# Kernel optimization log

Measured on AMD Instinct MI355X. Metric: run time of the kernel, lower is better.

## Reference

```python
import jax, jax.numpy as jnp
import numpy as np
from jax.scipy.special import digamma

# Dims (see init_kwargs): pose P=4 -> D=16, stem A=128, primary caps B=32,
# classes C=10, class-caps kernel K=6 (== primary feature map size), 3 routing iters.
P, D, A, B, C, K, ITER = 4, 16, 128, 32, 10, 6, 3
N = B * K * K                                    # input capsules routed to each class capsule
ALPHA0, KAPPA0, NU0 = 1.0, 1.0, float(D + 1)     # Dirichlet/Normal-Wishart priors (m0=0, Psi0=I, cov='diag')
BN_EPS, EPS = 1e-5, 1e-8


def conv2d(x, w, s):
    return jax.lax.conv_general_dilated(x, w, (s, s), 'VALID',
                                        dimension_numbers=('NCHW', 'OIHW', 'NCHW'))


def bn(x, gamma, beta, axes):
    # batch-norm with batch statistics (training-mode math)
    mu = x.mean(axes, keepdims=True)
    var = x.var(axes, keepdims=True)
    return (x - mu) * jax.lax.rsqrt(var + BN_EPS) * gamma + beta


def setup_inputs():
    key = jax.random.key(0)
    ks = jax.random.split(key, 4)
    f32 = jnp.float32
    x = jax.random.normal(ks[0], (128, 3, 32, 32), dtype=f32)
    conv1_w = jax.random.normal(ks[1], (A, 3, 5, 5), dtype=f32) * 0.1
    bn1_g = jnp.ones((A,), f32); bn1_b = jnp.zeros((A,), f32)
    prim_w = jax.random.normal(ks[2], (B * D + B, A, 3, 3), dtype=f32) * 0.05
    bna_g = jnp.ones((B,), f32); bna_b = jnp.zeros((B,), f32)
    bnp_g = jnp.ones((B,), f32); bnp_b = jnp.zeros((B,), f32)
    W_ij = jax.random.normal(ks[3], (B, C, K, K, P, P), dtype=f32) * 0.3
    return dict(x=x, conv1_w=conv1_w, bn1_g=bn1_g, bn1_b=bn1_b, prim_w=prim_w,
                bna_g=bna_g, bna_b=bna_b, bnp_g=bnp_g, bnp_b=bnp_b, W_ij=W_ij)


def _vb_stats(Ra, V):
    # Ra: (b,N,C) responsibility * input activation; V: (b,N,C,D) votes
    Nj = Ra.sum(1) + EPS                                         # (b,C)
    xbar = jnp.einsum('bnc,bncd->bcd', Ra, V) / Nj[..., None]    # weighted vote mean
    diff = V - xbar[:, None]
    sigma = jnp.einsum('bnc,bncd->bcd', Ra, diff * diff) / Nj[..., None]  # diag cov
    kappa = KAPPA0 + Nj
    m = Nj[..., None] * xbar / kappa[..., None]                  # posterior mean (m0 = 0)
    nu = NU0 + Nj
    Psi = 1.0 + Nj[..., None] * sigma + (KAPPA0 * Nj / kappa)[..., None] * xbar * xbar  # Psi0 = I (diag)
    return Nj, kappa, m, nu, Psi


def _expectations(Nj, nu, Psi, d_idx):
    alpha = ALPHA0 + Nj
    E_lnpi = digamma(alpha) - digamma(alpha.sum(-1, keepdims=True))
    E_lnLam = (digamma(0.5 * (nu[..., None] + 1.0 - d_idx)).sum(-1)
               + D * jnp.log(2.0) - jnp.log(Psi).sum(-1))
    return E_lnpi, E_lnLam


def reference(x, conv1_w, bn1_g, bn1_b, prim_w, bna_g, bna_b, bnp_g, bnp_b, W_ij):
    b = x.shape[0]
    # --- stem: Conv5x5/s2 + BN + ReLU ---
    h = conv2d(x, conv1_w, 2)                                    # (b,A,14,14)
    h = jax.nn.relu(bn(h, bn1_g[None, :, None, None], bn1_b[None, :, None, None], (0, 2, 3)))
    # --- primary capsules: Conv3x3/s2 -> poses + activations ---
    pc = conv2d(h, prim_w, 2)                                    # (b,B*D+B,6,6)
    poses, a = pc[:, :B * D], pc[:, B * D:]
    a = jax.nn.sigmoid(bn(a, bna_g[None, :, None, None], bna_b[None, :, None, None], (0, 2, 3)))
    poses = bn(poses.reshape(b, B, D, K, K),
               bnp_g[None, :, None, None, None], bnp_b[None, :, None, None, None], (0, 2, 3, 4))
    poses = poses.reshape(b, B, P, P, K, K)
    # --- class capsules: votes V = W_ij @ pose, kernel covers whole 6x6 map ---
    V = jnp.einsum('icxypq,biqrxy->bicxypr', W_ij, poses)        # (b,B,C,K,K,P,P)
    V = V.transpose(0, 1, 3, 4, 2, 5, 6).reshape(b, N, C, D)
    a_i = a.reshape(b, N)
    # --- variational Bayes routing (diag Normal-Wishart, ITER iterations) ---
    d_idx = jnp.arange(1, D + 1, dtype=x.dtype)
    R = jnp.full((b, N, C), 1.0 / C, dtype=x.dtype)
    for t in range(ITER):
        Nj, kappa, m, nu, Psi = _vb_stats(R * a_i[:, :, None], V)
        if t < ITER - 1:
            E_lnpi, E_lnLam = _expectations(Nj, nu, Psi, d_idx)
            dm = V - m[:, None]
            quad = D / kappa[:, None, :] + nu[:, None, :] * jnp.einsum('bncd,bcd->bnc', dm * dm, 1.0 / Psi)
            lnp = (E_lnpi[:, None] + 0.5 * E_lnLam[:, None]
                   - 0.5 * D * jnp.log(2.0 * jnp.pi) - 0.5 * quad)
            R = jax.nn.softmax(lnp, axis=-1)
    E_lnpi, E_lnLam = _expectations(Nj, nu, Psi, d_idx)
    logits = E_lnpi + 0.5 * E_lnLam                              # (b,C)
    yhat = jax.nn.sigmoid(bn(logits, 1.0, 0.0, (0,)))            # BatchNorm1d(affine=False)
    return yhat
```

## Files before the change

kernel.cpp:

```cpp
#include <hip/hip_runtime.h>
#include <hip/hip_bf16.h>

#define NB 128
#define AA 128
#define BB 32
#define CC 10
#define KK 6
#define DD 16
#define NN 1152
#define H1 14
#define CH2 544
#define NG 4608
#define KG 1152
#define MG 576

typedef short bfrag8 __attribute__((ext_vector_type(8)));
typedef float facc4 __attribute__((ext_vector_type(4)));

__device__ __forceinline__ unsigned short f2bf(float f) {
    unsigned u = __float_as_uint(f);
    u += 0x7FFF + ((u >> 16) & 1);
    return (unsigned short)(u >> 16);
}
__device__ __forceinline__ float bf2f(unsigned short s) {
    return __uint_as_float(((unsigned)s) << 16);
}

__global__ __launch_bounds__(256, 3) void k_conv1(const float* __restrict__ x,
                                                  const float* __restrict__ w,
                                                  float* __restrict__ h) {
    __shared__ __align__(16) float sX[3][7][32];
    __shared__ float sWf[AA * 75];
    const int p = blockIdx.x;
    const int b = blockIdx.y;
    const int tid = threadIdx.x;
    for (int j = tid; j < AA * 75; j += 256) sWf[j] = w[j];
    for (int j = tid; j < 3 * 7 * 32; j += 256) {
        int col = j & 31; int t2 = j >> 5; int row = t2 % 7; int ic = t2 / 7;
        sX[ic][row][col] = x[b * 3072 + ic * 1024 + (4 * p + row) * 32 + col];
    }
    __syncthreads();
    const int oc = tid & 127, ry = tid >> 7;
    const int r = 2 * p + ry;
    float acc[14];
#pragma unroll
    for (int j = 0; j < 14; ++j) acc[j] = 0.f;
    const float* wr = sWf + oc * 75;
#pragma unroll
    for (int ic = 0; ic < 3; ++ic) {
#pragma unroll
        for (int ky = 0; ky < 5; ++ky) {
            const float* xr = &sX[ic][2 * ry + ky][0];
            float row[32];
#pragma unroll
            for (int q = 0; q < 8; ++q) {
                float4 v = *reinterpret_cast<const float4*>(xr + q * 4);
                row[q * 4 + 0] = v.x; row[q * 4 + 1] = v.y;
                row[q * 4 + 2] = v.z; row[q * 4 + 3] = v.w;
            }
            float w0 = wr[ic * 25 + ky * 5 + 0];
            float w1 = wr[ic * 25 + ky * 5 + 1];
            float w2 = wr[ic * 25 + ky * 5 + 2];
            float w3 = wr[ic * 25 + ky * 5 + 3];
            float w4 = wr[ic * 25 + ky * 5 + 4];
#pragma unroll
            for (int ox = 0; ox < 14; ++ox) {
                float s = acc[ox];
                s = fmaf(row[2 * ox + 0], w0, s);
                s = fmaf(row[2 * ox + 1], w1, s);
                s = fmaf(row[2 * ox + 2], w2, s);
                s = fmaf(row[2 * ox + 3], w3, s);
                s = fmaf(row[2 * ox + 4], w4, s);
                acc[ox] = s;
            }
        }
    }
    float* out = h + ((size_t)(b * AA + oc) * 14 + r) * 14;
#pragma unroll
    for (int q = 0; q < 7; ++q)
        *reinterpret_cast<float2*>(out + q * 2) = make_float2(acc[q * 2], acc[q * 2 + 1]);
}

__device__ __forceinline__ void blk_reduce2(float& s, float& s2, int tid) {
#pragma unroll
    for (int o = 32; o > 0; o >>= 1) { s += __shfl_down(s, o); s2 += __shfl_down(s2, o); }
    __shared__ float ls[4], lq[4];
    int lane = tid & 63, wid = tid >> 6;
    if (lane == 0) { ls[wid] = s; lq[wid] = s2; }
    __syncthreads();
    if (tid == 0) {
        s = ls[0] + ls[1] + ls[2] + ls[3];
        s2 = lq[0] + lq[1] + lq[2] + lq[3];
    }
}

__global__ void k_bnstats1a(const float* __restrict__ h, float* __restrict__ part) {
    int c = blockIdx.x & 127, sl = blockIdx.x >> 7;
    int tid = threadIdx.x;
    float s = 0.f, s2 = 0.f;
    for (int j = tid; j < 16 * 196; j += 256) {
        int b = sl * 16 + j / 196, hw = j % 196;
        float v = h[((size_t)b * AA + c) * 196 + hw];
        s += v; s2 += v * v;
    }
    blk_reduce2(s, s2, tid);
    if (tid == 0) { part[c * 8 + sl] = s; part[1024 + c * 8 + sl] = s2; }
}

__global__ void k_bnfin1(const float* __restrict__ part, const float* __restrict__ g,
                         const float* __restrict__ be, float* __restrict__ bn1) {
    int c = threadIdx.x;
    float s = 0.f, s2 = 0.f;
#pragma unroll
    for (int sl = 0; sl < 8; ++sl) { s += part[c * 8 + sl]; s2 += part[1024 + c * 8 + sl]; }
    const float n = (float)(NB * 196);
    float mu = s / n;
    float var = s2 / n - mu * mu;
    float sc = g[c] * rsqrtf(var + 1e-5f);
    bn1[c] = sc;
    bn1[AA + c] = be[c] - mu * sc;
}

__global__ void k_prepw(const float* __restrict__ w, unsigned short* __restrict__ Ah,
                        unsigned short* __restrict__ Al) {
    int t = blockIdx.x * 256 + threadIdx.x;
    if (t >= MG * (KG / 8)) return;
    int row = t / (KG / 8), seg = t % (KG / 8);
    alignas(16) unsigned short hi[8], lo[8];
    if (row < CH2) {
        const float* src = w + (size_t)row * KG + seg * 8;
#pragma unroll
        for (int j = 0; j < 8; ++j) {
            float v = src[j];
            unsigned short hh = f2bf(v);
            hi[j] = hh;
            lo[j] = f2bf(v - bf2f(hh));
        }
    } else {
#pragma unroll
        for (int j = 0; j < 8; ++j) { hi[j] = 0; lo[j] = 0; }
    }
    *reinterpret_cast<uint4*>(Ah + (size_t)row * KG + seg * 8) = *reinterpret_cast<const uint4*>(hi);
    *reinterpret_cast<uint4*>(Al + (size_t)row * KG + seg * 8) = *reinterpret_cast<const uint4*>(lo);
}

__global__ void k_im2col(const float* __restrict__ h, const float* __restrict__ bn1,
                         unsigned short* __restrict__ Bh, unsigned short* __restrict__ Bl) {
    int t = blockIdx.x * 256 + threadIdx.x;
    if (t >= NG * (KG / 8)) return;
    int n = t / (KG / 8), seg = t % (KG / 8);
    int b = n / 36, xy = n % 36;
    int oy = xy / 6, ox = xy % 6;
    const float* hb = h + (size_t)b * (AA * 196) + (2 * oy) * 14 + 2 * ox;
    alignas(16) unsigned short hi[8], lo[8];
#pragma unroll
    for (int j = 0; j < 8; ++j) {
        int k = seg * 8 + j;
        int ic = k / 9, kk = k - ic * 9;
        int ky = kk / 3, kx = kk - ky * 3;
        float v = hb[ic * 196 + ky * 14 + kx];
        v = fmaxf(fmaf(v, bn1[ic], bn1[AA + ic]), 0.f);
        unsigned short hh = f2bf(v);
        hi[j] = hh;
        lo[j] = f2bf(v - bf2f(hh));
    }
    *reinterpret_cast<uint4*>(Bh + (size_t)n * KG + seg * 8) = *reinterpret_cast<const uint4*>(hi);
    *reinterpret_cast<uint4*>(Bl + (size_t)n * KG + seg * 8) = *reinterpret_cast<const uint4*>(lo);
}

__global__ __launch_bounds__(256, 4) void k_gemm(const unsigned short* __restrict__ Ah,
                                                 const unsigned short* __restrict__ Al,
                                                 const unsigned short* __restrict__ Bh,
                                                 const unsigned short* __restrict__ Bl,
                                                 float* __restrict__ pcT) {
    __shared__ alignas(16) unsigned short sAh[64][44], sAl[64][44];
    __shared__ alignas(16) unsigned short sBh[64][44], sBl[64][44];
    const int s = blockIdx.x;
    const int k8 = s & 7, j = s >> 3;
    const int jm = j / 9;
    const int y = k8 + 8 * jm;
    const int xg = j - 9 * jm;
    const int oc0 = xg * 64;
    const int n0 = y * 64;
    const int tid = threadIdx.x;
    const int lane = tid & 63, wv = tid >> 6;
    const int wm = wv >> 1, wn = wv & 1;
    const int quad = lane >> 4, r16 = lane & 15;
    const int srow = tid >> 2, sseg = tid & 3;

    facc4 acc[2][2] = {};
    const size_t gA = (size_t)(oc0 + srow) * KG + sseg * 8;
    const size_t gB = (size_t)(n0 + srow) * KG + sseg * 8;

    for (int ks = 0; ks < KG / 32; ++ks) {
        const int k0 = ks * 32;
        uint4 vAh = *reinterpret_cast<const uint4*>(Ah + gA + k0);
        uint4 vAl = *reinterpret_cast<const uint4*>(Al + gA + k0);
        uint4 vBh = *reinterpret_cast<const uint4*>(Bh + gB + k0);
        uint4 vBl = *reinterpret_cast<const uint4*>(Bl + gB + k0);
        __syncthreads();
        *reinterpret_cast<uint4*>(&sAh[srow][sseg * 8]) = vAh;
        *reinterpret_cast<uint4*>(&sAl[srow][sseg * 8]) = vAl;
        *reinterpret_cast<uint4*>(&sBh[srow][sseg * 8]) = vBh;
        *reinterpret_cast<uint4*>(&sBl[srow][sseg * 8]) = vBl;
        __syncthreads();
        bfrag8 ah[2], al[2], bh[2], bl[2];
#pragma unroll
        for (int i = 0; i < 2; ++i) {
            ah[i] = *reinterpret_cast<const bfrag8*>(&sAh[wm * 32 + i * 16 + r16][quad * 8]);
            al[i] = *reinterpret_cast<const bfrag8*>(&sAl[wm * 32 + i * 16 + r16][quad * 8]);
            bh[i] = *reinterpret_cast<const bfrag8*>(&sBh[wn * 32 + i * 16 + r16][quad * 8]);
            bl[i] = *reinterpret_cast<const bfrag8*>(&sBl[wn * 32 + i * 16 + r16][quad * 8]);
        }
#pragma unroll
        for (int i = 0; i < 2; ++i)
#pragma unroll
            for (int jj = 0; jj < 2; ++jj) {
                acc[i][jj] = __builtin_amdgcn_mfma_f32_16x16x32_bf16(ah[i], bh[jj], acc[i][jj], 0, 0, 0);
                acc[i][jj] = __builtin_amdgcn_mfma_f32_16x16x32_bf16(ah[i], bl[jj], acc[i][jj], 0, 0, 0);
                acc[i][jj] = __builtin_amdgcn_mfma_f32_16x16x32_bf16(al[i], bh[jj], acc[i][jj], 0, 0, 0);
            }
    }
#pragma unroll
    for (int i = 0; i < 2; ++i) {
        int oc_base = oc0 + wm * 32 + i * 16 + quad * 4;
        if (oc_base >= CH2) continue;
#pragma unroll
        for (int jj = 0; jj < 2; ++jj) {
            int n = n0 + wn * 32 + jj * 16 + r16;
            *reinterpret_cast<facc4*>(pcT + (size_t)n * CH2 + oc_base) = acc[i][jj];
        }
    }
}

__global__ void k_bnstats2a(const float* __restrict__ pcT, float* __restrict__ part) {
    int blk = blockIdx.x, tid = threadIdx.x;
    float s = 0.f, s2 = 0.f;
    if (blk < 256) {
        int i = blk >> 3, sl = blk & 7;
        for (int j = tid; j < 576 * 4; j += 256) {
            int row = sl * 576 + (j >> 2), q = j & 3;
            float4 v = *reinterpret_cast<const float4*>(pcT + (size_t)row * CH2 + i * 16 + q * 4);
            s += v.x + v.y + v.z + v.w;
            s2 += v.x * v.x + v.y * v.y + v.z * v.z + v.w * v.w;
        }
        blk_reduce2(s, s2, tid);
        if (tid == 0) { part[blk] = s; part[256 + blk] = s2; }
    } else {
        int t2 = blk - 256;
        int ch = t2 >> 1, sl = t2 & 1;
        for (int j = tid; j < 2304; j += 256) {
            int row = sl * 2304 + j;
            float v = pcT[(size_t)row * CH2 + BB * DD + ch];
            s += v; s2 += v * v;
        }
        blk_reduce2(s, s2, tid);
        if (tid == 0) { part[512 + t2] = s; part[576 + t2] = s2; }
    }
}

__global__ void k_bnfin2(const float* __restrict__ part,
                         const float* __restrict__ bna_g, const float* __restrict__ bna_b,
                         const float* __restrict__ bnp_g, const float* __restrict__ bnp_b,
                         float* __restrict__ bn2) {
    int t = threadIdx.x;
    if (t < 32) {
        float s = 0.f, s2 = 0.f;
#pragma unroll
        for (int sl = 0; sl < 8; ++sl) { s += part[t * 8 + sl]; s2 += part[256 + t * 8 + sl]; }
        const float n = (float)(NB * DD * 36);
        float mu = s / n, var = s2 / n - mu * mu;
        float sc = bnp_g[t] * rsqrtf(var + 1e-5f);
        bn2[t] = sc; bn2[32 + t] = bnp_b[t] - mu * sc;
    } else {
        int ch = t - 32;
        float s = part[512 + ch * 2] + part[512 + ch * 2 + 1];
        float s2 = part[576 + ch * 2] + part[576 + ch * 2 + 1];
        const float n = (float)(NB * 36);
        float mu = s / n, var = s2 / n - mu * mu;
        float sc = bna_g[ch] * rsqrtf(var + 1e-5f);
        bn2[64 + ch] = sc; bn2[96 + ch] = bna_b[ch] - mu * sc;
    }
}

__device__ __forceinline__ float digammaf_(float x) {
    float r = 0.f;
    while (x < 6.f) { r -= 1.f / x; x += 1.f; }
    float xi = 1.f / x;
    float xi2 = xi * xi;
    return r + logf(x) - 0.5f * xi -
           xi2 * (0.0833333333f - xi2 * (0.0083333333f - xi2 * 0.0039682540f));
}

template <int FIRST>
__global__ __launch_bounds__(640) void k_routed(
    const float* __restrict__ pcT, const float* __restrict__ bn2,
    const float* __restrict__ Wij,
    const float* __restrict__ S0i, const float* __restrict__ S1i, const float* __restrict__ S2i,
    float* __restrict__ S0o, float* __restrict__ S1o, float* __restrict__ S2o) {
    const int b = blockIdx.x >> 1, half = blockIdx.x & 1;
    const int tid = threadIdx.x;
    const int c = tid >> 6, lane = tid & 63;
    __shared__ float sLnp[CC][66];
    __shared__ float sBn2[128];
    __shared__ __align__(16) float sP[64][20];
    __shared__ float sA[64];
    __shared__ float sM[CC][16], sGq[CC][16], sBase[CC];
    if (tid < 128) sBn2[tid] = bn2[tid];
    if (!FIRST && tid < 160) {
        int cc = tid >> 4, d = tid & 15;
        int bc = b * CC + cc;
        float njraw = S0i[bc] + S0i[NB * CC + bc];
        float nj = njraw + 1e-8f;
        float kappa = 1.f + nj;
        float nu = 17.f + nj;
        float s1 = S1i[bc * 16 + d] + S1i[(NB * CC + bc) * 16 + d];
        float s2v = S2i[bc * 16 + d] + S2i[(NB * CC + bc) * 16 + d];
        float xbar = s1 / nj;
        float sig = (s2v - 2.f * xbar * s1 + xbar * xbar * njraw) / nj;
        float Psi = 1.f + nj * sig + (nj / kappa) * xbar * xbar;
        sM[cc][d] = nj * xbar / kappa;
        sGq[cc][d] = 0.5f * nu / Psi;
        float term = digammaf_(0.5f * (nu + 1.f - (float)(d + 1))) - logf(Psi);
#pragma unroll
        for (int o = 8; o > 0; o >>= 1) term += __shfl_down(term, o, 16);
        if (d == 0) {
            float asum = 0.f;
#pragma unroll
            for (int k = 0; k < CC; ++k)
                asum += 1.f + S0i[b * CC + k] + S0i[NB * CC + b * CC + k] + 1e-8f;
            float elnlam = 16.f * 0.69314718056f + term;
            float elnpi = digammaf_(1.f + nj) - digammaf_(asum);
            float lb = elnpi + 0.5f * elnlam;
            sBase[cc] = lb - 8.f * 1.83787706641f - 8.f / kappa;
        }
    }
    __syncthreads();
    float mc[16], Gc[16], basec = 0.f;
    if (!FIRST) {
#pragma unroll
        for (int d = 0; d < 16; ++d) { mc[d] = sM[c][d]; Gc[d] = sGq[c][d]; }
        basec = sBase[c];
    }
    float s0 = 0.f, s1[16], s2[16];
#pragma unroll
    for (int d = 0; d < 16; ++d) { s1[d] = 0.f; s2[d] = 0.f; }

#pragma unroll 1
    for (int it = 0; it < 9; ++it) {
        if (tid < 256) {
            int r = tid >> 2, q = tid & 3;
            int n = half * 576 + it * 64 + r;
            int i = n / 36, xy = n - i * 36;
            int row = b * 36 + xy;
            float4 v = *reinterpret_cast<const float4*>(pcT + (size_t)row * CH2 + i * 16 + q * 4);
            float psc = sBn2[i], psh = sBn2[32 + i];
            v.x = fmaf(v.x, psc, psh); v.y = fmaf(v.y, psc, psh);
            v.z = fmaf(v.z, psc, psh); v.w = fmaf(v.w, psc, psh);
            *reinterpret_cast<float4*>(&sP[r][q * 4]) = v;
        } else if (tid < 320) {
            int r = tid - 256;
            int n = half * 576 + it * 64 + r;
            int i = n / 36, xy = n - i * 36;
            int row = b * 36 + xy;
            float va = fmaf(pcT[(size_t)row * CH2 + BB * DD + i], sBn2[64 + i], sBn2[96 + i]);
            sA[r] = 1.f / (1.f + expf(-va));
        }
        __syncthreads();
        const int n = half * 576 + it * 64 + lane;
        const int i = n / 36, xy = n - i * 36;
        const float4* wp = reinterpret_cast<const float4*>(Wij + (((size_t)i * CC + c) * 36 + xy) * 16);
        alignas(16) float P[16], W[16];
        *reinterpret_cast<float4*>(&P[0])  = *reinterpret_cast<const float4*>(&sP[lane][0]);
        *reinterpret_cast<float4*>(&P[4])  = *reinterpret_cast<const float4*>(&sP[lane][4]);
        *reinterpret_cast<float4*>(&P[8])  = *reinterpret_cast<const float4*>(&sP[lane][8]);
        *reinterpret_cast<float4*>(&P[12]) = *reinterpret_cast<const float4*>(&sP[lane][12]);
        *reinterpret_cast<float4*>(&W[0])  = wp[0];
        *reinterpret_cast<float4*>(&W[4])  = wp[1];
        *reinterpret_cast<float4*>(&W[8])  = wp[2];
        *reinterpret_cast<float4*>(&W[12]) = wp[3];
        float V[16];
#pragma unroll
        for (int p = 0; p < 4; ++p)
#pragma unroll
            for (int r = 0; r < 4; ++r)
                V[p * 4 + r] = W[p * 4 + 0] * P[0 + r] + W[p * 4 + 1] * P[4 + r] +
                               W[p * 4 + 2] * P[8 + r] + W[p * 4 + 3] * P[12 + r];
        float av = sA[lane];
        float wgt;
        if (FIRST) {
            wgt = 0.1f * av;
            __syncthreads();
        } else {
            float q = 0.f;
#pragma unroll
            for (int d = 0; d < 16; ++d) {
                float dm = V[d] - mc[d];
                q = fmaf(dm * dm, Gc[d], q);
            }
            float lnp = basec - q;
            sLnp[c][lane] = lnp;
            __syncthreads();
            float mx = -1e30f;
#pragma unroll
            for (int cc = 0; cc < CC; ++cc) mx = fmaxf(mx, sLnp[cc][lane]);
            float ssum = 0.f;
#pragma unroll
            for (int cc = 0; cc < CC; ++cc) ssum += expf(sLnp[cc][lane] - mx);
            wgt = expf(lnp - mx) / ssum * av;
        }
        s0 += wgt;
#pragma unroll
        for (int d = 0; d < 16; ++d) {
            float wv = wgt * V[d];
            s1[d] += wv;
            s2[d] = fmaf(wv, V[d], s2[d]);
        }
    }
#pragma unroll
    for (int o = 32; o > 0; o >>= 1) {
        s0 += __shfl_down(s0, o);
#pragma unroll
        for (int k = 0; k < 16; ++k) {
            s1[k] += __shfl_down(s1[k], o);
            s2[k] += __shfl_down(s2[k], o);
        }
    }
    if (lane == 0) {
        int idx = half * (NB * CC) + b * CC + c;
        S0o[idx] = s0;
#pragma unroll
        for (int k = 0; k < 16; ++k) { S1o[idx * 16 + k] = s1[k]; S2o[idx * 16 + k] = s2[k]; }
    }
}

__global__ void k_expect_final(const float* __restrict__ S0p, const float* __restrict__ S1p,
                               const float* __restrict__ S2p, float* __restrict__ logits) {
    int b = blockIdx.x;
    int c = threadIdx.x;
    __shared__ float alph[CC];
    float njraw = 0.f;
    if (c < CC) {
        njraw = S0p[b * CC + c] + S0p[NB * CC + b * CC + c];
        alph[c] = 1.f + njraw + 1e-8f;
    }
    __syncthreads();
    if (c < CC) {
        int bc = b * CC + c;
        float nj = njraw + 1e-8f;
        float asum = 0.f;
#pragma unroll
        for (int k = 0; k < CC; ++k) asum += alph[k];
        float kappa = 1.f + nj;
        float nu = 17.f + nj;
        float S0 = njraw;
        float elnlam = 16.f * 0.69314718056f;
        for (int d = 0; d < 16; ++d) {
            float s1 = S1p[bc * 16 + d] + S1p[(NB * CC + bc) * 16 + d];
            float s2v = S2p[bc * 16 + d] + S2p[(NB * CC + bc) * 16 + d];
            float xbar = s1 / nj;
            float sig = (s2v - 2.f * xbar * s1 + xbar * xbar * S0) / nj;
            float Psi = 1.f + nj * sig + (nj / kappa) * xbar * xbar;
            elnlam += digammaf_(0.5f * (nu + 1.f - (float)(d + 1))) - logf(Psi);
        }
        float elnpi = digammaf_(1.f + nj) - digammaf_(asum);
        logits[bc] = elnpi + 0.5f * elnlam;
    }
}

__global__ void k_final(const float* __restrict__ logits, float* __restrict__ out) {
    int c = blockIdx.x;
    int b = threadIdx.x;
    float v = logits[b * CC + c];
    float s = v, s2 = v * v;
#pragma unroll
    for (int o = 32; o > 0; o >>= 1) { s += __shfl_down(s, o); s2 += __shfl_down(s2, o); }
    __shared__ float ls[2], lq[2];
    int lane = b & 63, wid = b >> 6;
    if (lane == 0) { ls[wid] = s; lq[wid] = s2; }
    __syncthreads();
    float mu = (ls[0] + ls[1]) * (1.f / 128.f);
    float var = (lq[0] + lq[1]) * (1.f / 128.f) - mu * mu;
    out[b * CC + c] = 1.f / (1.f + expf(-(v - mu) * rsqrtf(var + 1e-5f)));
}

extern "C" void kernel_launch(void* const* d_in, const int* in_sizes, int n_in,
                              void* d_out, int out_size, void* d_ws, size_t ws_size,
                              hipStream_t stream) {
    (void)in_sizes; (void)n_in; (void)out_size; (void)ws_size;
    const float* x       = (const float*)d_in[0];
    const float* conv1_w = (const float*)d_in[1];
    const float* bn1_g   = (const float*)d_in[2];
    const float* bn1_b   = (const float*)d_in[3];
    const float* prim_w  = (const float*)d_in[4];
    const float* bna_g   = (const float*)d_in[5];
    const float* bna_b   = (const float*)d_in[6];
    const float* bnp_g   = (const float*)d_in[7];
    const float* bnp_b   = (const float*)d_in[8];
    const float* Wij     = (const float*)d_in[9];

    float* ws = (float*)d_ws;
    float* h   = ws;
    float* pcT = ws + 3211264;
    unsigned short* Bh = (unsigned short*)(ws + 5718016);
    unsigned short* Bl = (unsigned short*)(ws + 8372224);
    unsigned short* Ahp = (unsigned short*)(ws + 11026432);
    unsigned short* Alp = (unsigned short*)(ws + 11358208);
    float* bn1    = ws + 11689984;
    float* bn2    = ws + 11690240;
    float* S0a    = ws + 11690368;
    float* S1a    = ws + 11692928;
    float* S2a    = ws + 11733888;
    float* S0b    = ws + 11774848;
    float* S1b    = ws + 11777408;
    float* S2b    = ws + 11818368;
    float* logits = ws + 11859328;
    float* part1  = ws + 11860608;
    float* part2  = ws + 11862656;
    float* out    = (float*)d_out;

    k_conv1<<<dim3(7, 128), 256, 0, stream>>>(x, conv1_w, h);
    k_bnstats1a<<<1024, 256, 0, stream>>>(h, part1);
    k_bnfin1<<<1, 128, 0, stream>>>(part1, bn1_g, bn1_b, bn1);
    k_prepw<<<324, 256, 0, stream>>>(prim_w, Ahp, Alp);
    k_im2col<<<2592, 256, 0, stream>>>(h, bn1, Bh, Bl);
    k_gemm<<<648, 256, 0, stream>>>(Ahp, Alp, Bh, Bl, pcT);
    k_bnstats2a<<<320, 256, 0, stream>>>(pcT, part2);
    k_bnfin2<<<1, 64, 0, stream>>>(part2, bna_g, bna_b, bnp_g, bnp_b, bn2);

    k_routed<1><<<256, 640, 0, stream>>>(pcT, bn2, Wij, S0a, S1a, S2a, S0a, S1a, S2a);
    k_routed<0><<<256, 640, 0, stream>>>(pcT, bn2, Wij, S0a, S1a, S2a, S0b, S1b, S2b);
    k_routed<0><<<256, 640, 0, stream>>>(pcT, bn2, Wij, S0b, S1b, S2b, S0a, S1a, S2a);
    k_expect_final<<<128, 64, 0, stream>>>(S0a, S1a, S2a, logits);

    k_final<<<10, 128, 0, stream>>>(logits, out);
}
```

Baseline: 188.0 us.

## Fuse BN finalize kernels into consumers and prefetch next GEMM K-slice

The one-block BN finalize kernels are folded into their consumers: the bn1 scale and shift are computed per block in a combined weight-prep and im2col kernel, and the bn2 values are computed per block inside each routing kernel. Weight prep and im2col now run as a single launch split by block index. The GEMM loop also loads the next K-slice from global memory into registers while the current slice is multiplied, a register double buffer. Together these remove three kernel launches and hide some global load latency, at the cost of redundant per-block BN finalization and higher register pressure in the GEMM.

```diff
diff --git a/kernel.cpp b/kernel.cpp
--- a/kernel.cpp
+++ b/kernel.cpp
@@ -107,47 +107,49 @@
     if (tid == 0) { part[c * 8 + sl] = s; part[1024 + c * 8 + sl] = s2; }
 }
 
-__global__ void k_bnfin1(const float* __restrict__ part, const float* __restrict__ g,
-                         const float* __restrict__ be, float* __restrict__ bn1) {
-    int c = threadIdx.x;
-    float s = 0.f, s2 = 0.f;
-#pragma unroll
-    for (int sl = 0; sl < 8; ++sl) { s += part[c * 8 + sl]; s2 += part[1024 + c * 8 + sl]; }
-    const float n = (float)(NB * 196);
-    float mu = s / n;
-    float var = s2 / n - mu * mu;
-    float sc = g[c] * rsqrtf(var + 1e-5f);
-    bn1[c] = sc;
-    bn1[AA + c] = be[c] - mu * sc;
-}
-
-__global__ void k_prepw(const float* __restrict__ w, unsigned short* __restrict__ Ah,
-                        unsigned short* __restrict__ Al) {
-    int t = blockIdx.x * 256 + threadIdx.x;
-    if (t >= MG * (KG / 8)) return;
-    int row = t / (KG / 8), seg = t % (KG / 8);
-    alignas(16) unsigned short hi[8], lo[8];
-    if (row < CH2) {
-        const float* src = w + (size_t)row * KG + seg * 8;
-#pragma unroll
-        for (int j = 0; j < 8; ++j) {
-            float v = src[j];
-            unsigned short hh = f2bf(v);
-            hi[j] = hh;
-            lo[j] = f2bf(v - bf2f(hh));
-        }
-    } else {
-#pragma unroll
-        for (int j = 0; j < 8; ++j) { hi[j] = 0; lo[j] = 0; }
-    }
-    *reinterpret_cast<uint4*>(Ah + (size_t)row * KG + seg * 8) = *reinterpret_cast<const uint4*>(hi);
-    *reinterpret_cast<uint4*>(Al + (size_t)row * KG + seg * 8) = *reinterpret_cast<const uint4*>(lo);
-}
-
-__global__ void k_im2col(const float* __restrict__ h, const float* __restrict__ bn1,
-                         unsigned short* __restrict__ Bh, unsigned short* __restrict__ Bl) {
-    int t = blockIdx.x * 256 + threadIdx.x;
-    if (t >= NG * (KG / 8)) return;
+__global__ void k_pim(const float* __restrict__ w, const float* __restrict__ h,
+                      const float* __restrict__ part1,
+                      const float* __restrict__ bn1_g, const float* __restrict__ bn1_b,
+                      unsigned short* __restrict__ Ah, unsigned short* __restrict__ Al,
+                      unsigned short* __restrict__ Bh, unsigned short* __restrict__ Bl) {
+    const int blk = blockIdx.x;
+    const int tid = threadIdx.x;
+    if (blk < 324) {
+        int t = blk * 256 + tid;
+        int row = t / (KG / 8), seg = t % (KG / 8);
+        alignas(16) unsigned short hi[8], lo[8];
+        if (row < CH2) {
+            const float* src = w + (size_t)row * KG + seg * 8;
+#pragma unroll
+            for (int j = 0; j < 8; ++j) {
+                float v = src[j];
+                unsigned short hh = f2bf(v);
+                hi[j] = hh;
+                lo[j] = f2bf(v - bf2f(hh));
+            }
+        } else {
+#pragma unroll
+            for (int j = 0; j < 8; ++j) { hi[j] = 0; lo[j] = 0; }
+        }
+        *reinterpret_cast<uint4*>(Ah + (size_t)row * KG + seg * 8) = *reinterpret_cast<const uint4*>(hi);
+        *reinterpret_cast<uint4*>(Al + (size_t)row * KG + seg * 8) = *reinterpret_cast<const uint4*>(lo);
+        return;
+    }
+    __shared__ float sBn1[2 * AA];
+    if (tid < AA) {
+        int c = tid;
+        float s = 0.f, s2 = 0.f;
+#pragma unroll
+        for (int sl = 0; sl < 8; ++sl) { s += part1[c * 8 + sl]; s2 += part1[1024 + c * 8 + sl]; }
+        const float n = (float)(NB * 196);
+        float mu = s / n;
+        float var = s2 / n - mu * mu;
+        float sc = bn1_g[c] * rsqrtf(var + 1e-5f);
+        sBn1[c] = sc;
+        sBn1[AA + c] = bn1_b[c] - mu * sc;
+    }
+    __syncthreads();
+    int t = (blk - 324) * 256 + tid;
     int n = t / (KG / 8), seg = t % (KG / 8);
     int b = n / 36, xy = n % 36;
     int oy = xy / 6, ox = xy % 6;
@@ -159,7 +161,7 @@
         int ic = k / 9, kk = k - ic * 9;
         int ky = kk / 3, kx = kk - ky * 3;
         float v = hb[ic * 196 + ky * 14 + kx];
-        v = fmaxf(fmaf(v, bn1[ic], bn1[AA + ic]), 0.f);
+        v = fmaxf(fmaf(v, sBn1[ic], sBn1[AA + ic]), 0.f);
         unsigned short hh = f2bf(v);
         hi[j] = hh;
         lo[j] = f2bf(v - bf2f(hh));
@@ -192,18 +194,25 @@
     const size_t gA = (size_t)(oc0 + srow) * KG + sseg * 8;
     const size_t gB = (size_t)(n0 + srow) * KG + sseg * 8;
 
+    uint4 vAh = *reinterpret_cast<const uint4*>(Ah + gA);
+    uint4 vAl = *reinterpret_cast<const uint4*>(Al + gA);
+    uint4 vBh = *reinterpret_cast<const uint4*>(Bh + gB);
+    uint4 vBl = *reinterpret_cast<const uint4*>(Bl + gB);
+
     for (int ks = 0; ks < KG / 32; ++ks) {
-        const int k0 = ks * 32;
-        uint4 vAh = *reinterpret_cast<const uint4*>(Ah + gA + k0);
-        uint4 vAl = *reinterpret_cast<const uint4*>(Al + gA + k0);
-        uint4 vBh = *reinterpret_cast<const uint4*>(Bh + gB + k0);
-        uint4 vBl = *reinterpret_cast<const uint4*>(Bl + gB + k0);
         __syncthreads();
         *reinterpret_cast<uint4*>(&sAh[srow][sseg * 8]) = vAh;
         *reinterpret_cast<uint4*>(&sAl[srow][sseg * 8]) = vAl;
         *reinterpret_cast<uint4*>(&sBh[srow][sseg * 8]) = vBh;
         *reinterpret_cast<uint4*>(&sBl[srow][sseg * 8]) = vBl;
         __syncthreads();
+        if (ks + 1 < KG / 32) {
+            const int k0n = (ks + 1) * 32;
+            vAh = *reinterpret_cast<const uint4*>(Ah + gA + k0n);
+            vAl = *reinterpret_cast<const uint4*>(Al + gA + k0n);
+            vBh = *reinterpret_cast<const uint4*>(Bh + gB + k0n);
+            vBl = *reinterpret_cast<const uint4*>(Bl + gB + k0n);
+        }
         bfrag8 ah[2], al[2], bh[2], bl[2];
 #pragma unroll
         for (int i = 0; i < 2; ++i) {
@@ -259,30 +268,6 @@
     }
 }
 
-__global__ void k_bnfin2(const float* __restrict__ part,
-                         const float* __restrict__ bna_g, const float* __restrict__ bna_b,
-                         const float* __restrict__ bnp_g, const float* __restrict__ bnp_b,
-                         float* __restrict__ bn2) {
-    int t = threadIdx.x;
-    if (t < 32) {
-        float s = 0.f, s2 = 0.f;
-#pragma unroll
-        for (int sl = 0; sl < 8; ++sl) { s += part[t * 8 + sl]; s2 += part[256 + t * 8 + sl]; }
-        const float n = (float)(NB * DD * 36);
-        float mu = s / n, var = s2 / n - mu * mu;
-        float sc = bnp_g[t] * rsqrtf(var + 1e-5f);
-        bn2[t] = sc; bn2[32 + t] = bnp_b[t] - mu * sc;
-    } else {
-        int ch = t - 32;
-        float s = part[512 + ch * 2] + part[512 + ch * 2 + 1];
-        float s2 = part[576 + ch * 2] + part[576 + ch * 2 + 1];
-        const float n = (float)(NB * 36);
-        float mu = s / n, var = s2 / n - mu * mu;
-        float sc = bna_g[ch] * rsqrtf(var + 1e-5f);
-        bn2[64 + ch] = sc; bn2[96 + ch] = bna_b[ch] - mu * sc;
-    }
-}
-
 __device__ __forceinline__ float digammaf_(float x) {
     float r = 0.f;
     while (x < 6.f) { r -= 1.f / x; x += 1.f; }
@@ -294,7 +279,9 @@
 
 template <int FIRST>
 __global__ __launch_bounds__(640) void k_routed(
-    const float* __restrict__ pcT, const float* __restrict__ bn2,
+    const float* __restrict__ pcT, const float* __restrict__ part2,
+    const float* __restrict__ bna_g, const float* __restrict__ bna_b,
+    const float* __restrict__ bnp_g, const float* __restrict__ bnp_b,
     const float* __restrict__ Wij,
     const float* __restrict__ S0i, const float* __restrict__ S1i, const float* __restrict__ S2i,
     float* __restrict__ S0o, float* __restrict__ S1o, float* __restrict__ S2o) {
@@ -306,7 +293,25 @@
     __shared__ __align__(16) float sP[64][20];
     __shared__ float sA[64];
     __shared__ float sM[CC][16], sGq[CC][16], sBase[CC];
-    if (tid < 128) sBn2[tid] = bn2[tid];
+    if (tid < 64) {
+        if (tid < 32) {
+            float s = 0.f, s2 = 0.f;
+#pragma unroll
+            for (int sl = 0; sl < 8; ++sl) { s += part2[tid * 8 + sl]; s2 += part2[256 + tid * 8 + sl]; }
+            const float n = (float)(NB * DD * 36);
+            float mu = s / n, var = s2 / n - mu * mu;
+            float sc = bnp_g[tid] * rsqrtf(var + 1e-5f);
+            sBn2[tid] = sc; sBn2[32 + tid] = bnp_b[tid] - mu * sc;
+        } else {
+            int ch = tid - 32;
+            float s = part2[512 + ch * 2] + part2[512 + ch * 2 + 1];
+            float s2 = part2[576 + ch * 2] + part2[576 + ch * 2 + 1];
+            const float n = (float)(NB * 36);
+            float mu = s / n, var = s2 / n - mu * mu;
+            float sc = bna_g[ch] * rsqrtf(var + 1e-5f);
+            sBn2[64 + ch] = sc; sBn2[96 + ch] = bna_b[ch] - mu * sc;
+        }
+    }
     if (!FIRST && tid < 160) {
         int cc = tid >> 4, d = tid & 15;
         int bc = b * CC + cc;
@@ -506,8 +511,6 @@
     unsigned short* Bl = (unsigned short*)(ws + 8372224);
     unsigned short* Ahp = (unsigned short*)(ws + 11026432);
     unsigned short* Alp = (unsigned short*)(ws + 11358208);
-    float* bn1    = ws + 11689984;
-    float* bn2    = ws + 11690240;
     float* S0a    = ws + 11690368;
     float* S1a    = ws + 11692928;
     float* S2a    = ws + 11733888;
@@ -521,16 +524,16 @@
 
     k_conv1<<<dim3(7, 128), 256, 0, stream>>>(x, conv1_w, h);
     k_bnstats1a<<<1024, 256, 0, stream>>>(h, part1);
-    k_bnfin1<<<1, 128, 0, stream>>>(part1, bn1_g, bn1_b, bn1);
-    k_prepw<<<324, 256, 0, stream>>>(prim_w, Ahp, Alp);
-    k_im2col<<<2592, 256, 0, stream>>>(h, bn1, Bh, Bl);
+    k_pim<<<2916, 256, 0, stream>>>(prim_w, h, part1, bn1_g, bn1_b, Ahp, Alp, Bh, Bl);
     k_gemm<<<648, 256, 0, stream>>>(Ahp, Alp, Bh, Bl, pcT);
     k_bnstats2a<<<320, 256, 0, stream>>>(pcT, part2);
-    k_bnfin2<<<1, 64, 0, stream>>>(part2, bna_g, bna_b, bnp_g, bnp_b, bn2);
-
-    k_routed<1><<<256, 640, 0, stream>>>(pcT, bn2, Wij, S0a, S1a, S2a, S0a, S1a, S2a);
-    k_routed<0><<<256, 640, 0, stream>>>(pcT, bn2, Wij, S0a, S1a, S2a, S0b, S1b, S2b);
-    k_routed<0><<<256, 640, 0, stream>>>(pcT, bn2, Wij, S0b, S1b, S2b, S0a, S1a, S2a);
+
+    k_routed<1><<<256, 640, 0, stream>>>(pcT, part2, bna_g, bna_b, bnp_g, bnp_b, Wij,
+                                         S0a, S1a, S2a, S0a, S1a, S2a);
+    k_routed<0><<<256, 640, 0, stream>>>(pcT, part2, bna_g, bna_b, bnp_g, bnp_b, Wij,
+                                         S0a, S1a, S2a, S0b, S1b, S2b);
+    k_routed<0><<<256, 640, 0, stream>>>(pcT, part2, bna_g, bna_b, bnp_g, bnp_b, Wij,
+                                         S0b, S1b, S2b, S0a, S1a, S2a);
     k_expect_final<<<128, 64, 0, stream>>>(S0a, S1a, S2a, logits);
 
     k_final<<<10, 128, 0, stream>>>(logits, out);
```

After: 178.2 us. 5.2% less time.
